# Kernel optimization log

Hardware: AMD Instinct MI355X
Metric: run time of the kernel (lower is better)

Reference implementation:

```python
import jax, jax.numpy as jnp
import numpy as np

H, D, G, P = 8, 64, 64, 3
ROPE_BASE = 10000.0

def _gelu(x):
    return jax.nn.gelu(x, approximate=False)  # torch nn.GELU default (erf)

def setup_inputs() -> dict:
    key = jax.random.key(0)
    ks = jax.random.split(key, 20)
    B, N, C = 2, 32768, 256
    inner = H * D
    s = 0.02
    inp = {
        'x': jax.random.normal(ks[0], (B, N, C), jnp.float32),
        'pos': jax.random.uniform(ks[1], (B, N, P), jnp.float32),
        'gumbel_u': jax.random.uniform(ks[2], (B, H, N, G), jnp.float32),
        'Wx': jax.random.normal(ks[3], (C, inner), jnp.float32) * s,
        'bx': jnp.zeros((inner,), jnp.float32),
        'W1': jax.random.normal(ks[4], (D, G), jnp.float32) * s,   # proj_temperature[0]
        'b1': jnp.zeros((G,), jnp.float32),
        'W2': jax.random.normal(ks[5], (G, 1), jnp.float32) * s,   # proj_temperature[2]
        'b2': jnp.zeros((1,), jnp.float32),
        'bias': jnp.full((1, H, 1, 1), 0.5, jnp.float32),
        'Wr': jax.random.normal(ks[6], (2 * P, D), jnp.float32) * s,  # rope_projection
        'br': jnp.zeros((D,), jnp.float32),
        'Ws': jax.random.normal(ks[7], (D, G), jnp.float32) * s,   # in_project_slice
        'bs': jnp.zeros((G,), jnp.float32),
        'Wq': jax.random.normal(ks[8], (D, D), jnp.float32) * s,
        'Wk': jax.random.normal(ks[9], (D, D), jnp.float32) * s,
        'Wv': jax.random.normal(ks[10], (D, D), jnp.float32) * s,
        'Wg1': jax.random.normal(ks[11], (2 * D, D), jnp.float32) * s,  # attn_gate[0]
        'bg1': jnp.zeros((D,), jnp.float32),
        'Wg2': jax.random.normal(ks[12], (D, D), jnp.float32) * s,      # attn_gate[2]
        'bg2': jnp.zeros((D,), jnp.float32),
        'Wo': jax.random.normal(ks[13], (inner, C), jnp.float32) * s,   # to_out
        'bo': jnp.zeros((C,), jnp.float32),
    }
    return inp

def reference(x, pos, gumbel_u, Wx, bx, W1, b1, W2, b2, bias, Wr, br, Ws, bs,
              Wq, Wk, Wv, Wg1, bg1, Wg2, bg2, Wo, bo):
    B, N, C = x.shape
    dt = x.dtype
    # project and split heads: [B,H,N,D]
    x_mid = (x @ Wx + bx).reshape(B, N, H, D).transpose(0, 2, 1, 3)
    # RoPE features: sin/cos of pos * inv_freq, projected to dim_head
    inv_freq = jnp.exp(-jnp.arange(P, dtype=dt) * jnp.log(jnp.asarray(ROPE_BASE, dt)) / P)
    ang = pos[..., :P] * inv_freq                                  # [B,N,P]
    rope_feat = jnp.concatenate([jnp.sin(ang), jnp.cos(ang)], -1)  # [B,N,2P]
    x_mid = x_mid + (rope_feat @ Wr + br)[:, None]                 # broadcast over heads
    # per-token temperature, clamped
    temp = _gelu(_gelu(x_mid @ W1 + b1) @ W2 + b2) + bias          # [B,H,N,1]
    temp = jnp.maximum(temp, 0.01)
    # gumbel-softmax slice weights (soft, hard=False)
    logits = x_mid @ Ws + bs                                       # [B,H,N,G]
    gnoise = -jnp.log(-jnp.log(gumbel_u + 1e-8) + 1e-8)
    sw = jax.nn.softmax((logits + gnoise) / temp, axis=-1)
    # pool N tokens into G slice tokens
    snorm = sw.sum(axis=2)                                         # [B,H,G]
    st = jnp.einsum('bhnc,bhng->bhgc', x_mid, sw) / (snorm + 1e-5)[..., None]
    # tiny SDPA over G learned tokens
    q, k, v = st @ Wq, st @ Wk, st @ Wv
    attn = jax.nn.softmax(jnp.einsum('bhgc,bhkc->bhgk', q, k) / jnp.sqrt(jnp.asarray(D, dt)), axis=-1)
    out_st = jnp.einsum('bhgk,bhkc->bhgc', attn, v)
    # sigmoid gate
    gate_in = jnp.concatenate([st, out_st], axis=-1)               # [B,H,G,2D]
    gate = jax.nn.sigmoid(jax.nn.silu(gate_in @ Wg1 + bg1) @ Wg2 + bg2)
    out_st = gate * out_st
    # broadcast slice tokens back to N tokens
    out_x = jnp.einsum('bhgc,bhng->bhnc', out_st, sw)
    out_x = out_x.transpose(0, 2, 1, 3).reshape(B, N, H * D)
    return out_x @ Wo + bo
```

## Files before the change

kernel.cpp:

```cpp
#include <hip/hip_runtime.h>
#include <math.h>

#define NSEQ 32768

using short8v = __attribute__((ext_vector_type(8))) short;
using f32x4   = __attribute__((ext_vector_type(4))) float;
#define MFMA16 __builtin_amdgcn_mfma_f32_16x16x32_bf16

__device__ __forceinline__ unsigned short f2bf(float f){
  union{float f; unsigned u;} v; v.f = f;
  return (unsigned short)((v.u + 0x7FFFu + ((v.u>>16)&1u))>>16);
}
__device__ __forceinline__ float bf2f(unsigned short h){
  union{unsigned u; float f;} v; v.u = ((unsigned)h)<<16; return v.f;
}
__device__ __forceinline__ void split2(float f, unsigned short* h, unsigned short* l){
  unsigned short hh = f2bf(f);
  *h = hh; *l = f2bf(f - bf2f(hh));
}
__device__ __forceinline__ float gelu_f(float x){
  return 0.5f*x*(1.f + erff(x*0.70710678118654752f));
}

__global__ __launch_bounds__(256) void k0_prep(const float* __restrict__ Wx,
    unsigned short* __restrict__ WxTH, unsigned short* __restrict__ WxTL)
{
  const int n = blockIdx.x;
  const int k = threadIdx.x;
  float v = Wx[(size_t)k*512 + n];
  unsigned short hh, ll; split2(v,&hh,&ll);
  WxTH[n*256+k]=hh; WxTL[n*256+k]=ll;
}

__global__ __launch_bounds__(256) void k0b_prep(
  const float* __restrict__ Wq, const float* __restrict__ Wk, const float* __restrict__ Wv,
  const float* __restrict__ Wg1, const float* __restrict__ Wg2, const float* __restrict__ Wo,
  const float* __restrict__ W1, const float* __restrict__ Ws,
  unsigned short* __restrict__ WqTH, unsigned short* __restrict__ WqTL,
  unsigned short* __restrict__ WkTH, unsigned short* __restrict__ WkTL,
  unsigned short* __restrict__ WvTH, unsigned short* __restrict__ WvTL,
  unsigned short* __restrict__ Wg1TH, unsigned short* __restrict__ Wg1TL,
  unsigned short* __restrict__ Wg2TH, unsigned short* __restrict__ Wg2TL,
  unsigned short* __restrict__ WoTH, unsigned short* __restrict__ WoTL,
  unsigned short* __restrict__ W1TH, unsigned short* __restrict__ W1TL,
  unsigned short* __restrict__ WsTH, unsigned short* __restrict__ WsTL)
{
  const int bx = blockIdx.x, t = threadIdx.x;
  unsigned short hh, ll;
  if (bx == 0){
    for (int i=0;i<16;i++){ int idx=i*256+t; int r=idx>>6, c=idx&63;
      split2(Wq[r*64+c],&hh,&ll); WqTH[c*64+r]=hh; WqTL[c*64+r]=ll;
      split2(Wk[r*64+c],&hh,&ll); WkTH[c*64+r]=hh; WkTL[c*64+r]=ll;
      split2(Wv[r*64+c],&hh,&ll); WvTH[c*64+r]=hh; WvTL[c*64+r]=ll;
    }
  } else if (bx == 1){
    for (int i=0;i<32;i++){ int idx=i*256+t; int r=idx>>6, c=idx&63;
      split2(Wg1[r*64+c],&hh,&ll); Wg1TH[c*128+r]=hh; Wg1TL[c*128+r]=ll;
    }
  } else if (bx == 2){
    for (int i=0;i<16;i++){ int idx=i*256+t; int r=idx>>6, c=idx&63;
      split2(Wg2[r*64+c],&hh,&ll); Wg2TH[c*64+r]=hh; Wg2TL[c*64+r]=ll;
      split2(W1[r*64+c],&hh,&ll);  W1TH[c*64+r]=hh;  W1TL[c*64+r]=ll;
      split2(Ws[r*64+c],&hh,&ll);  WsTH[c*64+r]=hh;  WsTL[c*64+r]=ll;
    }
  } else {
    int kb = (bx-3)*64;
    for (int i=0;i<64;i++){ int k = kb+i;
      split2(Wo[(size_t)k*256 + t],&hh,&ll);
      WoTH[(size_t)t*512 + k]=hh; WoTL[(size_t)t*512 + k]=ll;
    }
  }
}

__global__ __launch_bounds__(512,1) void k1_gemm_rope(
    const float* __restrict__ x, const float* __restrict__ pos,
    const unsigned short* __restrict__ WxTH, const unsigned short* __restrict__ WxTL,
    const float* __restrict__ bx,
    const float* __restrict__ Wr, const float* __restrict__ br,
    float* __restrict__ xmid)
{
  __shared__ unsigned short SA[2*128*128];
  __shared__ unsigned short SB[2*64*128];
  __shared__ float trig[128][8];
  const int tid = threadIdx.x;
  const int wave = tid>>6, lane = tid&63, l15 = lane&15, lq = lane>>4;
  const int m0 = blockIdx.x*128;

  if (tid < 128){
    int m = m0 + tid;
    float a0 = pos[m*3+0];
    float a1 = pos[m*3+1] * 0.046415888336127774f;
    float a2 = pos[m*3+2] * 0.002154434690031884f;
    trig[tid][0]=sinf(a0); trig[tid][1]=sinf(a1); trig[tid][2]=sinf(a2);
    trig[tid][3]=cosf(a0); trig[tid][4]=cosf(a1); trig[tid][5]=cosf(a2);
  }

  short8v aHr[8], aLr[8];
  {
    const int lm = tid>>2, lkq = (tid&3)*32;
    #pragma unroll
    for (int kh=0; kh<2; kh++){
      __syncthreads();
      const float* src = x + (size_t)(m0+lm)*256 + kh*128 + lkq;
      #pragma unroll
      for (int i=0;i<8;i++){
        float4 v = *(const float4*)(src + i*4);
        ushort4 hh, ll;
        split2(v.x,&hh.x,&ll.x); split2(v.y,&hh.y,&ll.y);
        split2(v.z,&hh.z,&ll.z); split2(v.w,&hh.w,&ll.w);
        int G = (lkq>>3) + (i>>1);
        int idx = lm*128 + (((G ^ (lm&15)))<<3) + ((i&1)<<2);
        *(ushort4*)&SA[idx] = hh;
        *(ushort4*)&SA[128*128 + idx] = ll;
      }
      __syncthreads();
      const int row = wave*16 + l15;
      #pragma unroll
      for (int ks=0; ks<4; ks++){
        int idx = row*128 + ((((ks<<2)+lq) ^ l15)<<3);
        aHr[kh*4+ks] = *(const short8v*)&SA[idx];
        aLr[kh*4+ks] = *(const short8v*)&SA[128*128 + idx];
      }
    }
  }

  float ropev[4][4];
  #pragma unroll
  for (int r=0;r<4;r++){
    int tk = wave*16 + lq*4 + r;
    float t0=trig[tk][0],t1=trig[tk][1],t2=trig[tk][2];
    float t3=trig[tk][3],t4=trig[tk][4],t5=trig[tk][5];
    #pragma unroll
    for (int j=0;j<4;j++){
      int d = j*16 + l15;
      float v = br[d];
      v = fmaf(t0, Wr[0*64+d], v);
      v = fmaf(t1, Wr[1*64+d], v);
      v = fmaf(t2, Wr[2*64+d], v);
      v = fmaf(t3, Wr[3*64+d], v);
      v = fmaf(t4, Wr[4*64+d], v);
      v = fmaf(t5, Wr[5*64+d], v);
      ropev[r][j] = v;
    }
  }

  const int bidx = m0 >> 15;
  const int nbase = (m0 & 32767) + wave*16 + lq*4;
  const int ln = tid>>3, lnkq = (tid&7)*16;

  for (int h=0; h<8; h++){
    f32x4 acc[4] = {};
    #pragma unroll
    for (int kh=0; kh<2; kh++){
      __syncthreads();
      {
        const unsigned short* sH = WxTH + (size_t)(h*64+ln)*256 + kh*128 + lnkq;
        const unsigned short* sL = WxTL + (size_t)(h*64+ln)*256 + kh*128 + lnkq;
        int g0 = lnkq>>3;
        int i0 = ln*128 + ((g0     ^ (ln&15))<<3);
        int i1 = ln*128 + (((g0+1) ^ (ln&15))<<3);
        *(uint4*)&SB[i0] = *(const uint4*)sH;
        *(uint4*)&SB[i1] = *(const uint4*)(sH+8);
        *(uint4*)&SB[64*128 + i0] = *(const uint4*)sL;
        *(uint4*)&SB[64*128 + i1] = *(const uint4*)(sL+8);
      }
      __syncthreads();
      #pragma unroll
      for (int ks=0; ks<4; ks++){
        short8v a_h = aHr[kh*4+ks], a_l = aLr[kh*4+ks];
        #pragma unroll
        for (int j=0;j<4;j++){
          int idx = (j*16+l15)*128 + ((((ks<<2)+lq) ^ l15)<<3);
          short8v b_h = *(const short8v*)&SB[idx];
          short8v b_l = *(const short8v*)&SB[64*128 + idx];
          acc[j] = MFMA16(a_h,b_h,acc[j],0,0,0);
          acc[j] = MFMA16(a_h,b_l,acc[j],0,0,0);
          acc[j] = MFMA16(a_l,b_h,acc[j],0,0,0);
        }
      }
    }
    #pragma unroll
    for (int j=0;j<4;j++){
      int col = j*16 + l15;
      float bxv = bx[h*64+col];
      #pragma unroll
      for (int r=0;r<4;r++){
        xmid[(((size_t)(bidx*8+h))*NSEQ + nbase + r)*64 + col] =
          acc[j][r] + bxv + ropev[r][j];
      }
    }
  }
}

__global__ __launch_bounds__(512,1) void k2_tile(
  const float* __restrict__ xmid, const float* __restrict__ gum,
  const unsigned short* __restrict__ W1TH, const unsigned short* __restrict__ W1TL,
  const float* __restrict__ b1,
  const float* __restrict__ W2, const float* __restrict__ b2,
  const float* __restrict__ biasp,
  const unsigned short* __restrict__ WsTH, const unsigned short* __restrict__ WsTL,
  const float* __restrict__ bs,
  unsigned* __restrict__ swT, float* __restrict__ part)
{
  __shared__ unsigned short XAh[128*72], XAl[128*72];
  __shared__ unsigned short XBh[64*128], XBl[64*128];
  __shared__ unsigned short W1h[64*72], W1l[64*72];
  __shared__ unsigned short Wsh[64*72], Wsl[64*72];
  __shared__ unsigned short swh[64*136], swl[64*136];
  __shared__ float snred[8*64];
  __shared__ float prm[200];

  const int tid = threadIdx.x;
  const int wave = tid>>6, lane = tid&63, l15 = lane&15, lq = lane>>4;
  const int bh = blockIdx.y, chunk = blockIdx.x, h = bh&7;
  const size_t rowbase = (size_t)bh*NSEQ;

  {
    const int g = tid>>3, c8 = (tid&7)*8;
    *(uint4*)&W1h[g*72+c8] = *(const uint4*)(W1TH + g*64 + c8);
    *(uint4*)&W1l[g*72+c8] = *(const uint4*)(W1TL + g*64 + c8);
    *(uint4*)&Wsh[g*72+c8] = *(const uint4*)(WsTH + g*64 + c8);
    *(uint4*)&Wsl[g*72+c8] = *(const uint4*)(WsTL + g*64 + c8);
  }
  if (tid<64){ prm[tid]=b1[tid]; prm[64+tid]=bs[tid]; prm[128+tid]=W2[tid]; }
  if (tid==64){ prm[192]=b2[0]; prm[193]=biasp[h]; }

  f32x4 acc2[2] = {};
  float snacc[4][4] = {};
  const int gt2 = wave>>1, dbase = (wave&1)*2;

  for (int sub=0; sub<4; ++sub){
    const int n0 = chunk*512 + sub*128;
    __syncthreads();
    {
      const int mq = (tid>>4)*4, dq = (tid&15)*4;
      const float* src = xmid + (rowbase + n0 + mq)*64 + dq;
      unsigned short hh[4][4], ll[4][4];
      #pragma unroll
      for (int i=0;i<4;i++){
        float4 v = *(const float4*)(src + i*64);
        split2(v.x,&hh[i][0],&ll[i][0]); split2(v.y,&hh[i][1],&ll[i][1]);
        split2(v.z,&hh[i][2],&ll[i][2]); split2(v.w,&hh[i][3],&ll[i][3]);
        ushort4 th; th.x=hh[i][0]; th.y=hh[i][1]; th.z=hh[i][2]; th.w=hh[i][3];
        ushort4 tl; tl.x=ll[i][0]; tl.y=ll[i][1]; tl.z=ll[i][2]; tl.w=ll[i][3];
        *(ushort4*)&XAh[(mq+i)*72 + dq] = th;
        *(ushort4*)&XAl[(mq+i)*72 + dq] = tl;
      }
      const int gm = mq>>3, mh = mq&7;
      #pragma unroll
      for (int j=0;j<4;j++){
        int d = dq+j;
        int base = d*128 + ((gm ^ (d&15))<<3) + mh;
        ushort4 th; th.x=hh[0][j]; th.y=hh[1][j]; th.z=hh[2][j]; th.w=hh[3][j];
        ushort4 tl; tl.x=ll[0][j]; tl.y=ll[1][j]; tl.z=ll[2][j]; tl.w=ll[3][j];
        *(ushort4*)&XBh[base] = th;
        *(ushort4*)&XBl[base] = tl;
      }
    }
    __syncthreads();

    const int mloc = wave*16 + l15;
    const float* grow = gum + (rowbase + n0 + mloc)*64;
    float4 gu[4];
    #pragma unroll
    for (int gt=0; gt<4; gt++) gu[gt] = *(const float4*)(grow + gt*16 + lq*4);

    f32x4 t1a[4] = {}, lga[4] = {};
    #pragma unroll
    for (int ks=0; ks<2; ks++){
      const int koff = ks*32 + lq*8;
      short8v xH = *(const short8v*)&XAh[(wave*16+l15)*72 + koff];
      short8v xL = *(const short8v*)&XAl[(wave*16+l15)*72 + koff];
      #pragma unroll
      for (int gt=0; gt<4; gt++){
        const int aoff = (gt*16+l15)*72 + koff;
        short8v wH = *(const short8v*)&W1h[aoff];
        short8v wL = *(const short8v*)&W1l[aoff];
        t1a[gt] = MFMA16(wH,xH,t1a[gt],0,0,0);
        t1a[gt] = MFMA16(wH,xL,t1a[gt],0,0,0);
        t1a[gt] = MFMA16(wL,xH,t1a[gt],0,0,0);
        short8v sH = *(const short8v*)&Wsh[aoff];
        short8v sL = *(const short8v*)&Wsl[aoff];
        lga[gt] = MFMA16(sH,xH,lga[gt],0,0,0);
        lga[gt] = MFMA16(sH,xL,lga[gt],0,0,0);
        lga[gt] = MFMA16(sL,xH,lga[gt],0,0,0);
      }
    }

    float p = 0.f;
    #pragma unroll
    for (int gt=0; gt<4; gt++)
      #pragma unroll
      for (int r=0;r<4;r++){
        int g = gt*16 + lq*4 + r;
        p += gelu_f(t1a[gt][r] + prm[g]) * prm[128+g];
      }
    p += __shfl_xor(p,16); p += __shfl_xor(p,32);
    float t2 = gelu_f(p + prm[192]);
    float rtemp = 1.f / fmaxf(t2 + prm[193], 0.01f);

    float z[4][4]; float mx = -1e30f;
    #pragma unroll
    for (int gt=0; gt<4; gt++){
      float guv[4] = {gu[gt].x, gu[gt].y, gu[gt].z, gu[gt].w};
      #pragma unroll
      for (int r=0;r<4;r++){
        int g = gt*16 + lq*4 + r;
        float gn = -__logf(-__logf(guv[r]+1e-8f)+1e-8f);
        float zz = (lga[gt][r] + prm[64+g] + gn)*rtemp;
        z[gt][r]=zz; mx = fmaxf(mx, zz);
      }
    }
    mx = fmaxf(mx, __shfl_xor(mx,16)); mx = fmaxf(mx, __shfl_xor(mx,32));
    float se = 0.f;
    #pragma unroll
    for (int gt=0; gt<4; gt++)
      #pragma unroll
      for (int r=0;r<4;r++){ float e = __expf(z[gt][r]-mx); z[gt][r]=e; se += e; }
    se += __shfl_xor(se,16); se += __shfl_xor(se,32);
    float inv = 1.f/se;
    #pragma unroll
    for (int gt=0; gt<4; gt++)
      #pragma unroll
      for (int r=0;r<4;r++){
        float swv = z[gt][r]*inv;
        snacc[gt][r] += swv;
        int g = gt*16 + lq*4 + r;
        unsigned short hh,ll; split2(swv,&hh,&ll);
        swh[g*136 + mloc] = hh; swl[g*136 + mloc] = ll;
      }
    __syncthreads();

    {
      const int g = tid>>3, mq = (tid&7)*16;
      #pragma unroll
      for (int i=0;i<4;i++){
        ushort4 hh = *(const ushort4*)&swh[g*136 + mq + i*4];
        ushort4 ll = *(const ushort4*)&swl[g*136 + mq + i*4];
        uint4 pk;
        pk.x = (unsigned)hh.x | ((unsigned)ll.x<<16);
        pk.y = (unsigned)hh.y | ((unsigned)ll.y<<16);
        pk.z = (unsigned)hh.z | ((unsigned)ll.z<<16);
        pk.w = (unsigned)hh.w | ((unsigned)ll.w<<16);
        *(uint4*)(swT + ((size_t)bh*64 + g)*NSEQ + n0 + mq + i*4) = pk;
      }
    }

    #pragma unroll
    for (int ks=0; ks<4; ks++){
      const int koff = ks*32 + lq*8;
      short8v aH = *(const short8v*)&swh[(gt2*16+l15)*136 + koff];
      short8v aL = *(const short8v*)&swl[(gt2*16+l15)*136 + koff];
      const int gran = ks*4 + lq;
      #pragma unroll
      for (int dt=0; dt<2; dt++){
        const int d = (dbase+dt)*16 + l15;
        const int boff = d*128 + ((gran ^ (d&15))<<3);
        short8v bH = *(const short8v*)&XBh[boff];
        short8v bL = *(const short8v*)&XBl[boff];
        acc2[dt] = MFMA16(aH,bH,acc2[dt],0,0,0);
        acc2[dt] = MFMA16(aH,bL,acc2[dt],0,0,0);
        acc2[dt] = MFMA16(aL,bH,acc2[dt],0,0,0);
      }
    }
  }

  float* pb = part + ((size_t)bh*64 + chunk)*4160;
  #pragma unroll
  for (int dt=0; dt<2; dt++)
    #pragma unroll
    for (int r=0;r<4;r++){
      int g = gt2*16 + lq*4 + r;
      int d = (dbase+dt)*16 + l15;
      pb[g*64 + d] = acc2[dt][r];
    }
  #pragma unroll
  for (int gt=0; gt<4; gt++)
    #pragma unroll
    for (int r=0;r<4;r++){
      float v = snacc[gt][r];
      v += __shfl_xor(v,1); v += __shfl_xor(v,2);
      v += __shfl_xor(v,4); v += __shfl_xor(v,8);
      if (l15==0) snred[wave*64 + gt*16 + lq*4 + r] = v;
    }
  __syncthreads();
  if (tid < 64){
    float s = 0.f;
    #pragma unroll
    for (int w=0; w<8; w++) s += snred[w*64 + tid];
    pb[4096 + tid] = s;
  }
}

__global__ __launch_bounds__(256) void k3a_reduce(
    const float* __restrict__ part, float* __restrict__ stred)
{
  const int bh = blockIdx.x;
  const int i = blockIdx.y*256 + threadIdx.x;
  if (i >= 4160) return;
  const float* pb = part + (size_t)bh*64*4160 + i;
  float s[8] = {};
  #pragma unroll 2
  for (int c=0; c<64; c+=8)
    #pragma unroll
    for (int j=0;j<8;j++) s[j] += pb[(size_t)(c+j)*4160];
  stred[bh*4160 + i] = ((s[0]+s[1])+(s[2]+s[3])) + ((s[4]+s[5])+(s[6]+s[7]));
}

__global__ __launch_bounds__(256) void k3b_slice(
    const float* __restrict__ stred,
    const unsigned short* __restrict__ WqTH, const unsigned short* __restrict__ WqTL,
    const unsigned short* __restrict__ WkTH, const unsigned short* __restrict__ WkTL,
    const unsigned short* __restrict__ WvTH, const unsigned short* __restrict__ WvTL,
    const unsigned short* __restrict__ Wg1TH, const unsigned short* __restrict__ Wg1TL,
    const unsigned short* __restrict__ Wg2TH, const unsigned short* __restrict__ Wg2TL,
    const unsigned short* __restrict__ WoTH, const unsigned short* __restrict__ WoTL,
    const float* __restrict__ bg1, const float* __restrict__ bg2,
    unsigned* __restrict__ MtP)
{
  __shared__ unsigned short stH[64*72], stL[64*72];
  __shared__ unsigned short qH[64*72],  qL[64*72];
  __shared__ unsigned short kH[64*72],  kL[64*72];
  __shared__ unsigned short vTH[64*72], vTL[64*72];
  __shared__ unsigned short pH[64*72],  pL[64*72];
  __shared__ unsigned short oH[64*72],  oL[64*72];
  __shared__ unsigned short h1H[64*72], h1L[64*72];
  __shared__ unsigned short gH[64*72],  gL[64*72];
  __shared__ float snl[64];

  const int tid = threadIdx.x;
  const int wave = tid>>6, lane = tid&63, l15 = lane&15, lq = lane>>4;
  const int bh = blockIdx.x, h = bh&7;
  const int grow = wave*16 + lq*4;

  if (tid < 64) snl[tid] = stred[bh*4160 + 4096 + tid] + 1e-5f;
  __syncthreads();
  {
    const int g = tid>>2, doff = (tid&3)*16;
    const float sn = snl[g];
    #pragma unroll
    for (int i=0;i<4;i++){
      float4 v = *(const float4*)(stred + bh*4160 + g*64 + doff + i*4);
      ushort4 hh, ll;
      split2(v.x/sn,&hh.x,&ll.x); split2(v.y/sn,&hh.y,&ll.y);
      split2(v.z/sn,&hh.z,&ll.z); split2(v.w/sn,&hh.w,&ll.w);
      *(ushort4*)&stH[g*72 + doff + i*4] = hh;
      *(ushort4*)&stL[g*72 + doff + i*4] = ll;
    }
  }
  __syncthreads();

  {
    f32x4 aq[4]={}, ak[4]={}, av[4]={};
    #pragma unroll
    for (int ks=0; ks<2; ks++){
      const int koff = ks*32 + lq*8;
      short8v sH = *(const short8v*)&stH[(wave*16+l15)*72 + koff];
      short8v sL = *(const short8v*)&stL[(wave*16+l15)*72 + koff];
      #pragma unroll
      for (int j=0;j<4;j++){
        const int boff = (j*16+l15)*64 + koff;
        short8v bH, bL;
        bH = *(const short8v*)(WqTH+boff); bL = *(const short8v*)(WqTL+boff);
        aq[j]=MFMA16(sH,bH,aq[j],0,0,0); aq[j]=MFMA16(sH,bL,aq[j],0,0,0); aq[j]=MFMA16(sL,bH,aq[j],0,0,0);
        bH = *(const short8v*)(WkTH+boff); bL = *(const short8v*)(WkTL+boff);
        ak[j]=MFMA16(sH,bH,ak[j],0,0,0); ak[j]=MFMA16(sH,bL,ak[j],0,0,0); ak[j]=MFMA16(sL,bH,ak[j],0,0,0);
        bH = *(const short8v*)(WvTH+boff); bL = *(const short8v*)(WvTL+boff);
        av[j]=MFMA16(sH,bH,av[j],0,0,0); av[j]=MFMA16(sH,bL,av[j],0,0,0); av[j]=MFMA16(sL,bH,av[j],0,0,0);
      }
    }
    #pragma unroll
    for (int j=0;j<4;j++){
      #pragma unroll
      for (int r=0;r<4;r++){
        unsigned short hh,ll;
        split2(aq[j][r],&hh,&ll); qH[(grow+r)*72 + j*16+l15]=hh; qL[(grow+r)*72 + j*16+l15]=ll;
        split2(ak[j][r],&hh,&ll); kH[(grow+r)*72 + j*16+l15]=hh; kL[(grow+r)*72 + j*16+l15]=ll;
        split2(av[j][r],&hh,&ll); vTH[(j*16+l15)*72 + grow+r]=hh; vTL[(j*16+l15)*72 + grow+r]=ll;
      }
    }
  }
  __syncthreads();

  {
    f32x4 sc[4]={};
    #pragma unroll
    for (int ks=0; ks<2; ks++){
      const int koff = ks*32 + lq*8;
      short8v aHf = *(const short8v*)&qH[(wave*16+l15)*72 + koff];
      short8v aLf = *(const short8v*)&qL[(wave*16+l15)*72 + koff];
      #pragma unroll
      for (int jt=0; jt<4; jt++){
        const int boff = (jt*16+l15)*72 + koff;
        short8v bH = *(const short8v*)&kH[boff];
        short8v bL = *(const short8v*)&kL[boff];
        sc[jt]=MFMA16(aHf,bH,sc[jt],0,0,0); sc[jt]=MFMA16(aHf,bL,sc[jt],0,0,0); sc[jt]=MFMA16(aLf,bH,sc[jt],0,0,0);
      }
    }
    #pragma unroll
    for (int r=0;r<4;r++){
      float s0=sc[0][r]*0.125f, s1=sc[1][r]*0.125f, s2=sc[2][r]*0.125f, s3=sc[3][r]*0.125f;
      float mx = fmaxf(fmaxf(s0,s1),fmaxf(s2,s3));
      mx=fmaxf(mx,__shfl_xor(mx,1)); mx=fmaxf(mx,__shfl_xor(mx,2));
      mx=fmaxf(mx,__shfl_xor(mx,4)); mx=fmaxf(mx,__shfl_xor(mx,8));
      float e0=__expf(s0-mx), e1=__expf(s1-mx), e2=__expf(s2-mx), e3=__expf(s3-mx);
      float se = e0+e1+e2+e3;
      se+=__shfl_xor(se,1); se+=__shfl_xor(se,2); se+=__shfl_xor(se,4); se+=__shfl_xor(se,8);
      float inv = 1.f/se;
      sc[0][r]=e0*inv; sc[1][r]=e1*inv; sc[2][r]=e2*inv; sc[3][r]=e3*inv;
    }
    #pragma unroll
    for (int jt=0; jt<4; jt++)
      #pragma unroll
      for (int r=0;r<4;r++){
        unsigned short hh,ll; split2(sc[jt][r],&hh,&ll);
        pH[(grow+r)*72 + jt*16+l15]=hh; pL[(grow+r)*72 + jt*16+l15]=ll;
      }
  }
  __syncthreads();

  f32x4 os[4] = {};
  {
    #pragma unroll
    for (int ks=0; ks<2; ks++){
      const int koff = ks*32 + lq*8;
      short8v aHf = *(const short8v*)&pH[(wave*16+l15)*72 + koff];
      short8v aLf = *(const short8v*)&pL[(wave*16+l15)*72 + koff];
      #pragma unroll
      for (int dt=0; dt<4; dt++){
        const int boff = (dt*16+l15)*72 + koff;
        short8v bH = *(const short8v*)&vTH[boff];
        short8v bL = *(const short8v*)&vTL[boff];
        os[dt]=MFMA16(aHf,bH,os[dt],0,0,0); os[dt]=MFMA16(aHf,bL,os[dt],0,0,0); os[dt]=MFMA16(aLf,bH,os[dt],0,0,0);
      }
    }
    #pragma unroll
    for (int dt=0; dt<4; dt++)
      #pragma unroll
      for (int r=0;r<4;r++){
        unsigned short hh,ll; split2(os[dt][r],&hh,&ll);
        oH[(grow+r)*72 + dt*16+l15]=hh; oL[(grow+r)*72 + dt*16+l15]=ll;
      }
  }
  __syncthreads();

  {
    f32x4 ha[4] = {};
    #pragma unroll
    for (int ks=0; ks<4; ks++){
      const int koff2 = (ks&1)*32 + lq*8;
      short8v aHf, aLf;
      if (ks<2){ aHf = *(const short8v*)&stH[(wave*16+l15)*72 + koff2];
                 aLf = *(const short8v*)&stL[(wave*16+l15)*72 + koff2]; }
      else     { aHf = *(const short8v*)&oH[(wave*16+l15)*72 + koff2];
                 aLf = *(const short8v*)&oL[(wave*16+l15)*72 + koff2]; }
      #pragma unroll
      for (int dt=0; dt<4; dt++){
        const int boff = (dt*16+l15)*128 + ks*32 + lq*8;
        short8v bH = *(const short8v*)(Wg1TH+boff);
        short8v bL = *(const short8v*)(Wg1TL+boff);
        ha[dt]=MFMA16(aHf,bH,ha[dt],0,0,0); ha[dt]=MFMA16(aHf,bL,ha[dt],0,0,0); ha[dt]=MFMA16(aLf,bH,ha[dt],0,0,0);
      }
    }
    #pragma unroll
    for (int dt=0; dt<4; dt++){
      float bg = bg1[dt*16+l15];
      #pragma unroll
      for (int r=0;r<4;r++){
        float s = ha[dt][r] + bg;
        float sv = s/(1.f+__expf(-s));
        unsigned short hh,ll; split2(sv,&hh,&ll);
        h1H[(grow+r)*72 + dt*16+l15]=hh; h1L[(grow+r)*72 + dt*16+l15]=ll;
      }
    }
  }
  __syncthreads();

  {
    f32x4 ga[4] = {};
    #pragma unroll
    for (int ks=0; ks<2; ks++){
      const int koff = ks*32 + lq*8;
      short8v aHf = *(const short8v*)&h1H[(wave*16+l15)*72 + koff];
      short8v aLf = *(const short8v*)&h1L[(wave*16+l15)*72 + koff];
      #pragma unroll
      for (int dt=0; dt<4; dt++){
        const int boff = (dt*16+l15)*64 + koff;
        short8v bH = *(const short8v*)(Wg2TH+boff);
        short8v bL = *(const short8v*)(Wg2TL+boff);
        ga[dt]=MFMA16(aHf,bH,ga[dt],0,0,0); ga[dt]=MFMA16(aHf,bL,ga[dt],0,0,0); ga[dt]=MFMA16(aLf,bH,ga[dt],0,0,0);
      }
    }
    #pragma unroll
    for (int dt=0; dt<4; dt++){
      float bg = bg2[dt*16+l15];
      #pragma unroll
      for (int r=0;r<4;r++){
        float gate = 1.f/(1.f+__expf(-(ga[dt][r]+bg)));
        float gv = gate * os[dt][r];
        unsigned short hh,ll; split2(gv,&hh,&ll);
        gH[(grow+r)*72 + dt*16+l15]=hh; gL[(grow+r)*72 + dt*16+l15]=ll;
      }
    }
  }
  __syncthreads();

  {
    f32x4 mac[16] = {};
    #pragma unroll
    for (int ks=0; ks<2; ks++){
      const int koff = ks*32 + lq*8;
      short8v aHf = *(const short8v*)&gH[(wave*16+l15)*72 + koff];
      short8v aLf = *(const short8v*)&gL[(wave*16+l15)*72 + koff];
      #pragma unroll
      for (int ct=0; ct<16; ct++){
        const size_t boff = (size_t)(ct*16+l15)*512 + h*64 + koff;
        short8v bH = *(const short8v*)(WoTH+boff);
        short8v bL = *(const short8v*)(WoTL+boff);
        mac[ct]=MFMA16(aHf,bH,mac[ct],0,0,0); mac[ct]=MFMA16(aHf,bL,mac[ct],0,0,0); mac[ct]=MFMA16(aLf,bH,mac[ct],0,0,0);
      }
    }
    #pragma unroll
    for (int ct=0; ct<16; ct++)
      #pragma unroll
      for (int r=0;r<4;r++){
        unsigned short hh,ll; split2(mac[ct][r],&hh,&ll);
        MtP[(size_t)bh*16384 + (size_t)(ct*16+l15)*64 + grow + r] =
          (unsigned)hh | ((unsigned)ll<<16);
      }
  }
}

__global__ __launch_bounds__(256,2) void k4_out(
  const unsigned* __restrict__ swT, const unsigned* __restrict__ MtP,
  const float* __restrict__ bo, float* __restrict__ out)
{
  __shared__ unsigned short AH[64*72], AL[64*72];
  __shared__ unsigned short BH[128*72], BL[128*72];
  const int tid = threadIdx.x;
  const int wave = tid>>6, lane = tid&63, l15 = lane&15, lq = lane>>4;
  const int m0 = blockIdx.x*64, c0 = blockIdx.y*128;
  const int b = m0>>15, nn = m0 & 32767;
  f32x4 acc[8] = {};

  for (int hh=0; hh<8; hh++){
    const int bhh = b*8 + hh;
    __syncthreads();
    {
      const int g = tid>>2, mq = (tid&3)*16;
      const unsigned* src = swT + ((size_t)bhh*64 + g)*NSEQ + nn + mq;
      #pragma unroll
      for (int i=0;i<4;i++){
        uint4 pv = *(const uint4*)(src + i*4);
        unsigned u[4]={pv.x,pv.y,pv.z,pv.w};
        #pragma unroll
        for (int j=0;j<4;j++){
          int m = mq + i*4 + j;
          AH[m*72+g] = (unsigned short)(u[j] & 0xFFFFu);
          AL[m*72+g] = (unsigned short)(u[j] >> 16);
        }
      }
      const int c = tid>>1, gq = (tid&1)*32;
      const unsigned* bsrc = MtP + (size_t)bhh*16384 + (size_t)(c0+c)*64 + gq;
      #pragma unroll
      for (int i=0;i<8;i++){
        uint4 pv = *(const uint4*)(bsrc + i*4);
        ushort4 hh4, ll4;
        hh4.x=(unsigned short)(pv.x&0xFFFFu); ll4.x=(unsigned short)(pv.x>>16);
        hh4.y=(unsigned short)(pv.y&0xFFFFu); ll4.y=(unsigned short)(pv.y>>16);
        hh4.z=(unsigned short)(pv.z&0xFFFFu); ll4.z=(unsigned short)(pv.z>>16);
        hh4.w=(unsigned short)(pv.w&0xFFFFu); ll4.w=(unsigned short)(pv.w>>16);
        *(ushort4*)&BH[c*72 + gq + i*4] = hh4;
        *(ushort4*)&BL[c*72 + gq + i*4] = ll4;
      }
    }
    __syncthreads();
    #pragma unroll
    for (int ks=0; ks<2; ks++){
      const int koff = ks*32 + lq*8;
      short8v aH = *(const short8v*)&AH[(wave*16+l15)*72 + koff];
      short8v aL = *(const short8v*)&AL[(wave*16+l15)*72 + koff];
      #pragma unroll
      for (int ct=0; ct<8; ct++){
        short8v bH = *(const short8v*)&BH[(ct*16+l15)*72 + koff];
        short8v bL = *(const short8v*)&BL[(ct*16+l15)*72 + koff];
        acc[ct] = MFMA16(aH,bH,acc[ct],0,0,0);
        acc[ct] = MFMA16(aH,bL,acc[ct],0,0,0);
        acc[ct] = MFMA16(aL,bH,acc[ct],0,0,0);
      }
    }
  }
  #pragma unroll
  for (int ct=0; ct<8; ct++)
    #pragma unroll
    for (int r=0;r<4;r++){
      int c = c0 + ct*16 + l15;
      out[(size_t)(m0 + wave*16 + lq*4 + r)*256 + c] = acc[ct][r] + bo[c];
    }
}

extern "C" void kernel_launch(void* const* d_in, const int* in_sizes, int n_in,
                              void* d_out, int out_size, void* d_ws, size_t ws_size,
                              hipStream_t stream) {
  (void)in_sizes; (void)n_in; (void)out_size;
  const float* x    = (const float*)d_in[0];
  const float* pos  = (const float*)d_in[1];
  const float* gum  = (const float*)d_in[2];
  const float* Wx   = (const float*)d_in[3];
  const float* bx   = (const float*)d_in[4];
  const float* W1   = (const float*)d_in[5];
  const float* b1   = (const float*)d_in[6];
  const float* W2   = (const float*)d_in[7];
  const float* b2   = (const float*)d_in[8];
  const float* bias = (const float*)d_in[9];
  const float* Wr   = (const float*)d_in[10];
  const float* br   = (const float*)d_in[11];
  const float* Ws   = (const float*)d_in[12];
  const float* bs   = (const float*)d_in[13];
  const float* Wq   = (const float*)d_in[14];
  const float* Wk   = (const float*)d_in[15];
  const float* Wv   = (const float*)d_in[16];
  const float* Wg1  = (const float*)d_in[17];
  const float* bg1  = (const float*)d_in[18];
  const float* Wg2  = (const float*)d_in[19];
  const float* bg2  = (const float*)d_in[20];
  const float* Wo   = (const float*)d_in[21];
  const float* bo   = (const float*)d_in[22];
  float* out = (float*)d_out;

  float*    xmid  = (float*)d_ws;
  unsigned* swT   = (unsigned*)(xmid + (size_t)33554432);
  float*    partp = (float*)(swT + (size_t)33554432);
  float*    stred = partp + (size_t)4259840;
  unsigned short* WxTH = (unsigned short*)(stred + (size_t)66560);
  unsigned short* WxTL  = WxTH + (size_t)131072;
  unsigned short* WqTH  = WxTL + (size_t)131072;
  unsigned short* WqTL  = WqTH + 4096;
  unsigned short* WkTH  = WqTL + 4096;
  unsigned short* WkTL  = WkTH + 4096;
  unsigned short* WvTH  = WkTL + 4096;
  unsigned short* WvTL  = WvTH + 4096;
  unsigned short* Wg1TH = WvTL + 4096;
  unsigned short* Wg1TL = Wg1TH + 8192;
  unsigned short* Wg2TH = Wg1TL + 8192;
  unsigned short* Wg2TL = Wg2TH + 4096;
  unsigned short* WoTH  = Wg2TL + 4096;
  unsigned short* WoTL  = WoTH + (size_t)131072;
  unsigned short* W1TH  = WoTL + (size_t)131072;
  unsigned short* W1TL  = W1TH + 4096;
  unsigned short* WsTH  = W1TL + 4096;
  unsigned short* WsTL  = WsTH + 4096;
  unsigned* MtP = (unsigned*)partp;
  const size_t need = ((size_t)33554432*2 + 4259840 + 66560)*4 + (size_t)589824*2;
  if (ws_size < need) return;

  k0_prep<<<512, 256, 0, stream>>>(Wx, WxTH, WxTL);
  k0b_prep<<<11, 256, 0, stream>>>(Wq, Wk, Wv, Wg1, Wg2, Wo, W1, Ws,
      WqTH,WqTL,WkTH,WkTL,WvTH,WvTL,Wg1TH,Wg1TL,Wg2TH,Wg2TL,WoTH,WoTL,W1TH,W1TL,WsTH,WsTL);
  k1_gemm_rope<<<512, 512, 0, stream>>>(x, pos, WxTH, WxTL, bx, Wr, br, xmid);
  k2_tile<<<dim3(64,16), 512, 0, stream>>>(xmid, gum, W1TH, W1TL, b1, W2, b2, bias, WsTH, WsTL, bs, swT, partp);
  k3a_reduce<<<dim3(16,17), 256, 0, stream>>>(partp, stred);
  k3b_slice<<<16, 256, 0, stream>>>(stred, WqTH,WqTL,WkTH,WkTL,WvTH,WvTL,
      Wg1TH,Wg1TL,Wg2TH,Wg2TL,WoTH,WoTL, bg1, bg2, MtP);
  k4_out<<<dim3(1024,2), 256, 0, stream>>>(swT, MtP, bo, out);
}
```

Baseline: 418.0 us.

## Shrink k2 tile to 256 threads with smaller LDS for two blocks per CU

```diff
diff --git a/kernel.cpp b/kernel.cpp
--- a/kernel.cpp
+++ b/kernel.cpp
@@ -192,7 +192,7 @@
   }
 }
 
-__global__ __launch_bounds__(512,1) void k2_tile(
+__global__ __launch_bounds__(256,2) void k2_tile(
   const float* __restrict__ xmid, const float* __restrict__ gum,
   const unsigned short* __restrict__ W1TH, const unsigned short* __restrict__ W1TL,
   const float* __restrict__ b1,
@@ -202,12 +202,11 @@
   const float* __restrict__ bs,
   unsigned* __restrict__ swT, float* __restrict__ part)
 {
-  __shared__ unsigned short XAh[128*72], XAl[128*72];
-  __shared__ unsigned short XBh[64*128], XBl[64*128];
+  __shared__ unsigned short XBh[64*72], XBl[64*72];
   __shared__ unsigned short W1h[64*72], W1l[64*72];
   __shared__ unsigned short Wsh[64*72], Wsl[64*72];
-  __shared__ unsigned short swh[64*136], swl[64*136];
-  __shared__ float snred[8*64];
+  __shared__ unsigned short swh[64*72], swl[64*72];
+  __shared__ float snred[4*64];
   __shared__ float prm[200];
 
   const int tid = threadIdx.x;
@@ -216,50 +215,57 @@
   const size_t rowbase = (size_t)bh*NSEQ;
 
   {
-    const int g = tid>>3, c8 = (tid&7)*8;
-    *(uint4*)&W1h[g*72+c8] = *(const uint4*)(W1TH + g*64 + c8);
-    *(uint4*)&W1l[g*72+c8] = *(const uint4*)(W1TL + g*64 + c8);
-    *(uint4*)&Wsh[g*72+c8] = *(const uint4*)(WsTH + g*64 + c8);
-    *(uint4*)&Wsl[g*72+c8] = *(const uint4*)(WsTL + g*64 + c8);
+    const int g = tid>>2, c16 = (tid&3)*16;
+    *(uint4*)&W1h[g*72+c16]   = *(const uint4*)(W1TH + g*64 + c16);
+    *(uint4*)&W1h[g*72+c16+8] = *(const uint4*)(W1TH + g*64 + c16 + 8);
+    *(uint4*)&W1l[g*72+c16]   = *(const uint4*)(W1TL + g*64 + c16);
+    *(uint4*)&W1l[g*72+c16+8] = *(const uint4*)(W1TL + g*64 + c16 + 8);
+    *(uint4*)&Wsh[g*72+c16]   = *(const uint4*)(WsTH + g*64 + c16);
+    *(uint4*)&Wsh[g*72+c16+8] = *(const uint4*)(WsTH + g*64 + c16 + 8);
+    *(uint4*)&Wsl[g*72+c16]   = *(const uint4*)(WsTL + g*64 + c16);
+    *(uint4*)&Wsl[g*72+c16+8] = *(const uint4*)(WsTL + g*64 + c16 + 8);
   }
   if (tid<64){ prm[tid]=b1[tid]; prm[64+tid]=bs[tid]; prm[128+tid]=W2[tid]; }
   if (tid==64){ prm[192]=b2[0]; prm[193]=biasp[h]; }
 
-  f32x4 acc2[2] = {};
+  f32x4 acc2[4] = {};
   float snacc[4][4] = {};
-  const int gt2 = wave>>1, dbase = (wave&1)*2;
-
-  for (int sub=0; sub<4; ++sub){
-    const int n0 = chunk*512 + sub*128;
+  const int mloc = wave*16 + l15;
+  const int mq = (tid>>4)*4, dq = (tid&15)*4;
+
+  for (int sub=0; sub<8; ++sub){
+    const int n0 = chunk*512 + sub*64;
     __syncthreads();
     {
-      const int mq = (tid>>4)*4, dq = (tid&15)*4;
       const float* src = xmid + (rowbase + n0 + mq)*64 + dq;
       unsigned short hh[4][4], ll[4][4];
       #pragma unroll
       for (int i=0;i<4;i++){
-        float4 v = *(const float4*)(src + i*64);
+        float4 v = *(const float4*)(src + (size_t)i*64);
         split2(v.x,&hh[i][0],&ll[i][0]); split2(v.y,&hh[i][1],&ll[i][1]);
         split2(v.z,&hh[i][2],&ll[i][2]); split2(v.w,&hh[i][3],&ll[i][3]);
-        ushort4 th; th.x=hh[i][0]; th.y=hh[i][1]; th.z=hh[i][2]; th.w=hh[i][3];
-        ushort4 tl; tl.x=ll[i][0]; tl.y=ll[i][1]; tl.z=ll[i][2]; tl.w=ll[i][3];
-        *(ushort4*)&XAh[(mq+i)*72 + dq] = th;
-        *(ushort4*)&XAl[(mq+i)*72 + dq] = tl;
-      }
-      const int gm = mq>>3, mh = mq&7;
+      }
       #pragma unroll
       for (int j=0;j<4;j++){
         int d = dq+j;
-        int base = d*128 + ((gm ^ (d&15))<<3) + mh;
         ushort4 th; th.x=hh[0][j]; th.y=hh[1][j]; th.z=hh[2][j]; th.w=hh[3][j];
         ushort4 tl; tl.x=ll[0][j]; tl.y=ll[1][j]; tl.z=ll[2][j]; tl.w=ll[3][j];
-        *(ushort4*)&XBh[base] = th;
-        *(ushort4*)&XBl[base] = tl;
+        *(ushort4*)&XBh[d*72 + mq] = th;
+        *(ushort4*)&XBl[d*72 + mq] = tl;
       }
     }
     __syncthreads();
 
-    const int mloc = wave*16 + l15;
+    float4 xf[4];
+    {
+      const float* xrow = xmid + (rowbase + n0 + mloc)*64;
+      #pragma unroll
+      for (int ks=0; ks<2; ks++){
+        const int koff = ks*32 + lq*8;
+        xf[ks*2]   = *(const float4*)(xrow + koff);
+        xf[ks*2+1] = *(const float4*)(xrow + koff + 4);
+      }
+    }
     const float* grow = gum + (rowbase + n0 + mloc)*64;
     float4 gu[4];
     #pragma unroll
@@ -269,8 +275,14 @@
     #pragma unroll
     for (int ks=0; ks<2; ks++){
       const int koff = ks*32 + lq*8;
-      short8v xH = *(const short8v*)&XAh[(wave*16+l15)*72 + koff];
-      short8v xL = *(const short8v*)&XAl[(wave*16+l15)*72 + koff];
+      float xv[8] = {xf[ks*2].x,xf[ks*2].y,xf[ks*2].z,xf[ks*2].w,
+                     xf[ks*2+1].x,xf[ks*2+1].y,xf[ks*2+1].z,xf[ks*2+1].w};
+      short8v xH, xL;
+      #pragma unroll
+      for (int j=0;j<8;j++){
+        unsigned short hh,ll; split2(xv[j],&hh,&ll);
+        xH[j]=(short)hh; xL[j]=(short)ll;
+      }
       #pragma unroll
       for (int gt=0; gt<4; gt++){
         const int aoff = (gt*16+l15)*72 + koff;
@@ -327,37 +339,35 @@
         snacc[gt][r] += swv;
         int g = gt*16 + lq*4 + r;
         unsigned short hh,ll; split2(swv,&hh,&ll);
-        swh[g*136 + mloc] = hh; swl[g*136 + mloc] = ll;
+        swh[g*72 + mloc] = hh; swl[g*72 + mloc] = ll;
       }
     __syncthreads();
 
     {
-      const int g = tid>>3, mq = (tid&7)*16;
+      const int g = tid>>2, mq2 = (tid&3)*16;
       #pragma unroll
       for (int i=0;i<4;i++){
-        ushort4 hh = *(const ushort4*)&swh[g*136 + mq + i*4];
-        ushort4 ll = *(const ushort4*)&swl[g*136 + mq + i*4];
+        ushort4 hh = *(const ushort4*)&swh[g*72 + mq2 + i*4];
+        ushort4 ll = *(const ushort4*)&swl[g*72 + mq2 + i*4];
         uint4 pk;
         pk.x = (unsigned)hh.x | ((unsigned)ll.x<<16);
         pk.y = (unsigned)hh.y | ((unsigned)ll.y<<16);
         pk.z = (unsigned)hh.z | ((unsigned)ll.z<<16);
         pk.w = (unsigned)hh.w | ((unsigned)ll.w<<16);
-        *(uint4*)(swT + ((size_t)bh*64 + g)*NSEQ + n0 + mq + i*4) = pk;
-      }
-    }
-
-    #pragma unroll
-    for (int ks=0; ks<4; ks++){
+        *(uint4*)(swT + ((size_t)bh*64 + g)*NSEQ + n0 + mq2 + i*4) = pk;
+      }
+    }
+
+    #pragma unroll
+    for (int ks=0; ks<2; ks++){
       const int koff = ks*32 + lq*8;
-      short8v aH = *(const short8v*)&swh[(gt2*16+l15)*136 + koff];
-      short8v aL = *(const short8v*)&swl[(gt2*16+l15)*136 + koff];
-      const int gran = ks*4 + lq;
-      #pragma unroll
-      for (int dt=0; dt<2; dt++){
-        const int d = (dbase+dt)*16 + l15;
-        const int boff = d*128 + ((gran ^ (d&15))<<3);
-        short8v bH = *(const short8v*)&XBh[boff];
-        short8v bL = *(const short8v*)&XBl[boff];
+      short8v aH = *(const short8v*)&swh[(wave*16+l15)*72 + koff];
+      short8v aL = *(const short8v*)&swl[(wave*16+l15)*72 + koff];
+      #pragma unroll
+      for (int dt=0; dt<4; dt++){
+        const int d = dt*16 + l15;
+        short8v bH = *(const short8v*)&XBh[d*72 + koff];
+        short8v bL = *(const short8v*)&XBl[d*72 + koff];
         acc2[dt] = MFMA16(aH,bH,acc2[dt],0,0,0);
         acc2[dt] = MFMA16(aH,bL,acc2[dt],0,0,0);
         acc2[dt] = MFMA16(aL,bH,acc2[dt],0,0,0);
@@ -367,11 +377,11 @@
 
   float* pb = part + ((size_t)bh*64 + chunk)*4160;
   #pragma unroll
-  for (int dt=0; dt<2; dt++)
+  for (int dt=0; dt<4; dt++)
     #pragma unroll
     for (int r=0;r<4;r++){
-      int g = gt2*16 + lq*4 + r;
-      int d = (dbase+dt)*16 + l15;
+      int g = wave*16 + lq*4 + r;
+      int d = dt*16 + l15;
       pb[g*64 + d] = acc2[dt][r];
     }
   #pragma unroll
@@ -387,7 +397,7 @@
   if (tid < 64){
     float s = 0.f;
     #pragma unroll
-    for (int w=0; w<8; w++) s += snred[w*64 + tid];
+    for (int w=0; w<4; w++) s += snred[w*64 + tid];
     pb[4096 + tid] = s;
   }
 }
@@ -758,7 +768,7 @@
   k0b_prep<<<11, 256, 0, stream>>>(Wq, Wk, Wv, Wg1, Wg2, Wo, W1, Ws,
       WqTH,WqTL,WkTH,WkTL,WvTH,WvTL,Wg1TH,Wg1TL,Wg2TH,Wg2TL,WoTH,WoTL,W1TH,W1TL,WsTH,WsTL);
   k1_gemm_rope<<<512, 512, 0, stream>>>(x, pos, WxTH, WxTL, bx, Wr, br, xmid);
-  k2_tile<<<dim3(64,16), 512, 0, stream>>>(xmid, gum, W1TH, W1TL, b1, W2, b2, bias, WsTH, WsTL, bs, swT, partp);
+  k2_tile<<<dim3(64,16), 256, 0, stream>>>(xmid, gum, W1TH, W1TL, b1, W2, b2, bias, WsTH, WsTL, bs, swT, partp);
   k3a_reduce<<<dim3(16,17), 256, 0, stream>>>(partp, stred);
   k3b_slice<<<16, 256, 0, stream>>>(stred, WqTH,WqTL,WkTH,WkTL,WvTH,WvTL,
       Wg1TH,Wg1TL,Wg2TH,Wg2TL,WoTH,WoTL, bg1, bg2, MtP);
```

Result: faster. 409.5 us (-2.0%).
